# Performance work log

Measured on AMD Instinct MI355X. Metric: run time of the kernel, lower is better.

## Reference

```python
import jax, jax.numpy as jnp
import numpy as np

S, LC = 4096, 16
N_WORD, N_CHAR = 100000, 128
CHAR_DIM, CHAR_HIDDEN = 64, 128
N_DIM, N_HIDDEN, N_TAG = 256, 512, 64


def setup_inputs() -> dict:
    key = jax.random.key(0)
    ks = jax.random.split(key, 16)
    rn = lambda k, shape, s=0.1: (jax.random.normal(k, shape, jnp.float32) * s)
    inp = {
        'char_emb': rn(ks[0], (N_CHAR, CHAR_DIM), 1.0),
        'char_Wih': rn(ks[1], (4 * CHAR_HIDDEN, CHAR_DIM)),
        'char_Whh': rn(ks[2], (4 * CHAR_HIDDEN, CHAR_HIDDEN)),
        'char_bih': rn(ks[3], (4 * CHAR_HIDDEN,)),
        'char_bhh': rn(ks[4], (4 * CHAR_HIDDEN,)),
        'word_emb': rn(ks[5], (N_WORD, N_DIM), 1.0),
        'Wih': rn(ks[6], (4 * N_HIDDEN, N_DIM + CHAR_HIDDEN)),
        'Whh': rn(ks[7], (4 * N_HIDDEN, N_HIDDEN)),
        'bih': rn(ks[8], (4 * N_HIDDEN,)),
        'bhh': rn(ks[9], (4 * N_HIDDEN,)),
        'W1': rn(ks[10], (N_TAG, N_HIDDEN)),
        'b1': rn(ks[11], (N_TAG,)),
        'x': jax.random.randint(ks[12], (S,), 0, N_WORD),
        'chars': jax.random.randint(ks[13], (S, LC), 0, N_CHAR),
        'char_lens': jax.random.randint(ks[14], (S,), 1, LC + 1),
    }
    return inp


def _lstm(xs, mask, Wih, Whh, bih, bhh):
    # xs: [T, B, In], mask: [T, B] bool. PyTorch gate order: i, f, g, o.
    T, B, _ = xs.shape
    H = Whh.shape[1]
    def step(carry, inp):
        h, c = carry
        x_t, m_t = inp
        g = x_t @ Wih.T + bih + h @ Whh.T + bhh  # [B, 4H]
        i, f, gg, o = jnp.split(g, 4, axis=-1)
        c_new = jax.nn.sigmoid(f) * c + jax.nn.sigmoid(i) * jnp.tanh(gg)
        h_new = jax.nn.sigmoid(o) * jnp.tanh(c_new)
        m = m_t[:, None]
        h2 = jnp.where(m, h_new, h)
        c2 = jnp.where(m, c_new, c)
        return (h2, c2), h2
    init = (jnp.zeros((B, H), xs.dtype), jnp.zeros((B, H), xs.dtype))
    (h_fin, _), hs = jax.lax.scan(step, init, (xs, mask))
    return hs, h_fin


def reference(char_emb, char_Wih, char_Whh, char_bih, char_bhh,
              word_emb, Wih, Whh, bih, bhh, W1, b1,
              x, chars, char_lens):
    # --- char-level LSTM, all S words batched (replaces per-word Python loop) ---
    cx = char_emb[chars]                      # [S, LC, char_dim]
    cx = jnp.transpose(cx, (1, 0, 2))         # [LC, S, char_dim]
    cmask = jnp.arange(LC)[:, None] < char_lens[None, :]  # [LC, S]
    _, char_h = _lstm(cx, cmask, char_Wih, char_Whh, char_bih, char_bhh)  # [S, char_hidden]

    # --- word-level LSTM over the sentence (batch 1, as in original) ---
    wx = word_emb[x]                          # [S, n_dim]
    feat = jnp.concatenate([wx, char_h], axis=-1)[:, None, :]  # [S, 1, n_dim+char_hidden]
    wmask = jnp.ones((feat.shape[0], 1), bool)
    hs, _ = _lstm(feat, wmask, Wih, Whh, bih, bhh)  # [S, 1, n_hidden]
    hs = hs[:, 0, :]

    logits = hs @ W1.T + b1                   # [S, n_tag]
    return jax.nn.log_softmax(logits, axis=-1)
```

## Files before the change

### kernel.cpp

```cpp
#include <hip/hip_runtime.h>
#include <hip/hip_bf16.h>


#define OFF_FLAG  0
#define OFF_CEMB  16
#define OFF_CWIH  8208
#define OFF_CBIH  40976
#define OFF_CBHH  41488
#define OFF_CWHH  42000
#define OFF_BIH   107536
#define OFF_BHH   109584
#define OFF_W1T   111632
#define OFF_CGE   144400
#define OFF_CH    209936
#define OFF_XP2   734224
#define OFF_HH    4928528

#define SENT 0xFFFFFFFFu

__device__ __forceinline__ float sigf(float x) { return 1.0f / (1.0f + __expf(-x)); }
__device__ __forceinline__ float tanh_f(float x) { return 2.0f * sigf(2.0f * x) - 1.0f; }
__device__ __forceinline__ float b2f_lo(unsigned u) { return __uint_as_float(u << 16); }
__device__ __forceinline__ float b2f_hi(unsigned u) { return __uint_as_float(u & 0xFFFF0000u); }

__global__ void detect_kernel(const unsigned* __restrict__ w, int* __restrict__ flagp) {
    unsigned v = w[threadIdx.x];
    unsigned e = (v >> 7) & 0xFF;
    int inr = (e >= 100 && e <= 140) ? 1 : 0;
    unsigned long long m = __ballot(inr);
    if (threadIdx.x == 0) flagp[0] = (__popcll(m) >= 56) ? 1 : 0;
}

__global__ void convf_kernel(const void* __restrict__ s, float* __restrict__ d,
                             int n, const int* __restrict__ flagp) {
    int i = blockIdx.x * 256 + threadIdx.x;
    if (i >= n) return;
    d[i] = flagp[0] ? __bfloat162float(((const __hip_bfloat16*)s)[i])
                    : ((const float*)s)[i];
}

__global__ void w1t_kernel(const void* __restrict__ W1, float* __restrict__ W1T,
                           const int* __restrict__ flagp) {
    int i = blockIdx.x * 256 + threadIdx.x;
    int j = i & 63, k = i >> 6;
    W1T[i] = flagp[0] ? __bfloat162float(((const __hip_bfloat16*)W1)[j * 512 + k])
                      : ((const float*)W1)[j * 512 + k];
}

__global__ void __launch_bounds__(256) cge_kernel(
    const float* __restrict__ cemb, const float* __restrict__ cWih,
    const float* __restrict__ cbih, const float* __restrict__ cbhh,
    float* __restrict__ cge)
{
    __shared__ float xe[64];
    int c = blockIdx.x, tid = threadIdx.x;
    if (tid < 64) xe[tid] = cemb[c * 64 + tid];
    __syncthreads();
#pragma unroll
    for (int rep = 0; rep < 2; ++rep) {
        int j = rep * 256 + tid;
        float acc = cbih[j] + cbhh[j];
#pragma unroll 8
        for (int k = 0; k < 64; ++k)
            acc += xe[k] * cWih[j * 64 + k];
        cge[c * 512 + j] = acc;
    }
}

__global__ void __launch_bounds__(256) char_lstm_kernel(
    const float* __restrict__ cge, const float* __restrict__ Whh,
    const int* __restrict__ chars, const int* __restrict__ lens,
    float* __restrict__ char_h)
{
    __shared__ float hls[16][128];
    int tid = threadIdx.x;
    int wl = tid >> 4, sl = tid & 15;
    int w = blockIdx.x * 16 + wl;
    int len = lens[w];
    const int* cw = chars + w * 16;
    float c[8];
#pragma unroll
    for (int q = 0; q < 8; ++q) { c[q] = 0.0f; hls[wl][sl * 8 + q] = 0.0f; }

    for (int t = 0; t < 16; ++t) {
        __syncthreads();
        int ch = cw[t];
        const float* xg = cge + ch * 512;
        float acc[4][8];
#pragma unroll
        for (int g = 0; g < 4; ++g)
#pragma unroll
            for (int q = 0; q < 8; ++q)
                acc[g][q] = xg[g * 128 + sl * 8 + q];

        const float4* h4 = (const float4*)hls[wl];
#pragma unroll
        for (int g = 0; g < 4; ++g) {
            const float4* wbase = ((const float4*)Whh) + (g * 128 + sl * 8) * 32;
            for (int k4 = 0; k4 < 32; ++k4) {
                float4 hv = h4[k4];
#pragma unroll
                for (int q = 0; q < 8; ++q) {
                    float4 wv = wbase[q * 32 + k4];
                    acc[g][q] += wv.x * hv.x + wv.y * hv.y + wv.z * hv.z + wv.w * hv.w;
                }
            }
        }
        __syncthreads();
        if (t < len) {
#pragma unroll
            for (int q = 0; q < 8; ++q) {
                float iv = sigf(acc[0][q]);
                float fv = sigf(acc[1][q]);
                float gv = tanh_f(acc[2][q]);
                float ov = sigf(acc[3][q]);
                c[q] = fv * c[q] + iv * gv;
                hls[wl][sl * 8 + q] = ov * tanh_f(c[q]);
            }
        }
    }
    __syncthreads();
#pragma unroll
    for (int q = 0; q < 8; ++q)
        char_h[w * 128 + sl * 8 + q] = hls[wl][sl * 8 + q];
}

__global__ void __launch_bounds__(256) xp2_kernel(
    const void* __restrict__ wemb, const int* __restrict__ x,
    const float* __restrict__ char_h, const void* __restrict__ Wraw,
    const float* __restrict__ bih, const float* __restrict__ bhh,
    __hip_bfloat16* __restrict__ xp2, const int* __restrict__ flagp)
{
    __shared__ float feat[16][384];
    int flag = flagp[0];
    int tid = threadIdx.x, tl = tid >> 4, sl = tid & 15;
    int t = blockIdx.x * 16 + tl;
    int xw = x[t];
    for (int idx = sl; idx < 384; idx += 16) {
        float v;
        if (idx < 256)
            v = flag ? __bfloat162float(((const __hip_bfloat16*)wemb)[(size_t)xw * 256 + idx])
                     : ((const float*)wemb)[(size_t)xw * 256 + idx];
        else
            v = char_h[t * 128 + (idx - 256)];
        feat[tl][idx] = v;
    }
    __syncthreads();

    const float4* f4 = (const float4*)feat[tl];
    for (int rb = 0; rb < 4; ++rb) {
        int r0 = rb * 512 + sl * 32;
        for (int qc = 0; qc < 4; ++qc) {
            int rr = r0 + qc * 8;
            float acc[8];
#pragma unroll
            for (int q = 0; q < 8; ++q)
                acc[q] = bih[rr + q] + bhh[rr + q];
            if (!flag) {
                const float4* wb = ((const float4*)Wraw) + (size_t)rr * 96;
                for (int k4 = 0; k4 < 96; ++k4) {
                    float4 fv = f4[k4];
#pragma unroll
                    for (int q = 0; q < 8; ++q) {
                        float4 wv = wb[q * 96 + k4];
                        acc[q] += wv.x * fv.x + wv.y * fv.y + wv.z * fv.z + wv.w * fv.w;
                    }
                }
            } else {
                const uint2* wb = ((const uint2*)Wraw) + (size_t)rr * 96;
                for (int k4 = 0; k4 < 96; ++k4) {
                    float4 fv = f4[k4];
#pragma unroll
                    for (int q = 0; q < 8; ++q) {
                        uint2 wv = wb[q * 96 + k4];
                        acc[q] += b2f_lo(wv.x) * fv.x + b2f_hi(wv.x) * fv.y
                                + b2f_lo(wv.y) * fv.z + b2f_hi(wv.y) * fv.w;
                    }
                }
            }
#pragma unroll
            for (int q = 0; q < 8; ++q)
                xp2[(size_t)t * 2048 + rr + q] = __float2bfloat16(acc[q]);
        }
    }
}

__global__ void __launch_bounds__(1024, 4) word_lstm_kernel(
    const __hip_bfloat16* __restrict__ xp2, const void* __restrict__ Whh_raw,
    float* __restrict__ h_hist, const int* __restrict__ flagp)
{
    __shared__ float hpad[2][576];
    __shared__ float hout[16];
    __shared__ int step_flag;
    int flag = flagp[0];
    int wg = blockIdx.x;
    int tid = threadIdx.x;
    int wave = tid >> 6, lane = tid & 63;
    int g = lane >> 4, kk = lane & 15;
    int slot = wg * 16 + wave;
    int grow = g * 512 + slot;

    float4 wreg[8];
    if (!flag) {
        const float4* wr = (const float4*)((const float*)Whh_raw + (size_t)grow * 512 + kk * 32);
#pragma unroll
        for (int i = 0; i < 8; ++i) wreg[i] = wr[i];
    } else {
        const uint2* wr = (const uint2*)((const unsigned short*)Whh_raw + (size_t)grow * 512 + kk * 32);
#pragma unroll
        for (int i = 0; i < 8; ++i) {
            uint2 u = wr[i];
            wreg[i] = make_float4(b2f_lo(u.x), b2f_hi(u.x), b2f_lo(u.y), b2f_hi(u.y));
        }
    }

    for (int i = tid; i < 576; i += 1024) hpad[0][i] = 0.0f;
    if (tid == 0) step_flag = 0;
    __syncthreads();

    unsigned* hview = (unsigned*)h_hist;
    float c = 0.0f;

    for (int t = 0; t < 4096; ++t) {
        float xv = __bfloat162float(xp2[(size_t)t * 2048 + grow]);

        unsigned ls = 0;
        while (__hip_atomic_load(&step_flag, __ATOMIC_ACQUIRE,
                                 __HIP_MEMORY_SCOPE_WORKGROUP) < t) {
            if (++ls > (1u << 24)) break;
        }

        const float4* h4 = (const float4*)(&hpad[t & 1][kk * 36]);
        float acc = 0.0f;
#pragma unroll
        for (int i = 0; i < 8; ++i) {
            float4 hv = h4[i];
            acc += wreg[i].x * hv.x + wreg[i].y * hv.y +
                   wreg[i].z * hv.z + wreg[i].w * hv.w;
        }
        acc += __shfl_xor(acc, 1);
        acc += __shfl_xor(acc, 2);
        acc += __shfl_xor(acc, 4);
        acc += __shfl_xor(acc, 8);
        float gvt = acc + xv;

        float iv = __shfl(gvt, kk);
        float fv = __shfl(gvt, 16 + kk);
        float gg = __shfl(gvt, 32 + kk);
        float ov = __shfl(gvt, 48 + kk);
        c = sigf(fv) * c + sigf(iv) * tanh_f(gg);
        float h = sigf(ov) * tanh_f(c);

        if (lane == 0) hout[wave] = h;
        __syncthreads();

        if (wave == 0) {
            if (lane < 16)
                __hip_atomic_store(hview + (size_t)t * 512 + wg * 16 + lane,
                                   __float_as_uint(hout[lane]),
                                   __ATOMIC_RELAXED, __HIP_MEMORY_SCOPE_AGENT);

            if (t < 4095) {
                unsigned v[8];
                if ((lane >> 1) == wg) {
#pragma unroll
                    for (int i = 0; i < 8; ++i)
                        v[i] = __float_as_uint(hout[(lane & 1) * 8 + i]);
                } else {
                    const unsigned* src = hview + (size_t)t * 512 + lane * 8;
                    unsigned spins = 0;
                    bool bail = false;
                    for (;;) {
#pragma unroll
                        for (int i = 0; i < 8; ++i)
                            v[i] = __hip_atomic_load(src + i, __ATOMIC_RELAXED,
                                                     __HIP_MEMORY_SCOPE_AGENT);
                        int ok = 1;
#pragma unroll
                        for (int i = 0; i < 8; ++i) ok &= (v[i] != SENT);
                        if (ok) break;
                        if (++spins > (1u << 22)) { bail = true; break; }
                    }
                    if (bail) {
#pragma unroll
                        for (int i = 0; i < 8; ++i) v[i] = __float_as_uint(12345.0f);
                    }
                }
                float* dst = &hpad[(t + 1) & 1][(lane >> 2) * 36 + (lane & 3) * 8];
                ((float4*)dst)[0] = make_float4(__uint_as_float(v[0]), __uint_as_float(v[1]),
                                                __uint_as_float(v[2]), __uint_as_float(v[3]));
                ((float4*)dst)[1] = make_float4(__uint_as_float(v[4]), __uint_as_float(v[5]),
                                                __uint_as_float(v[6]), __uint_as_float(v[7]));
                __hip_atomic_store(&step_flag, t + 1, __ATOMIC_RELEASE,
                                   __HIP_MEMORY_SCOPE_WORKGROUP);
            }
        }
    }
}

__global__ void __launch_bounds__(64) out_kernel(
    const float* __restrict__ h_hist, const float* __restrict__ W1T,
    const void* __restrict__ b1raw, void* __restrict__ out,
    const int* __restrict__ flagp)
{
    __shared__ float hb[512];
    int flag = flagp[0];
    int t = blockIdx.x, j = threadIdx.x;
    const float4* src = (const float4*)(h_hist + (size_t)t * 512);
    ((float4*)hb)[j * 2] = src[j * 2];
    ((float4*)hb)[j * 2 + 1] = src[j * 2 + 1];
    __syncthreads();

    float acc = flag ? __bfloat162float(((const __hip_bfloat16*)b1raw)[j])
                     : ((const float*)b1raw)[j];
#pragma unroll 8
    for (int k = 0; k < 512; ++k)
        acc += hb[k] * W1T[k * 64 + j];

    float m = acc;
#pragma unroll
    for (int o = 32; o; o >>= 1) m = fmaxf(m, __shfl_xor(m, o));
    float e = __expf(acc - m);
    float s = e;
#pragma unroll
    for (int o = 32; o; o >>= 1) s += __shfl_xor(s, o);
    float r = acc - m - __logf(s);
    if (flag) ((__hip_bfloat16*)out)[t * 64 + j] = __float2bfloat16(r);
    else      ((float*)out)[t * 64 + j] = r;
}

extern "C" void kernel_launch(void* const* d_in, const int* in_sizes, int n_in,
                              void* d_out, int out_size, void* d_ws, size_t ws_size,
                              hipStream_t stream)
{
    (void)in_sizes; (void)n_in; (void)out_size; (void)ws_size;
    const void* char_emb = d_in[0];
    const void* char_Wih = d_in[1];
    const void* char_Whh = d_in[2];
    const void* char_bih = d_in[3];
    const void* char_bhh = d_in[4];
    const void* word_emb = d_in[5];
    const void* Wih      = d_in[6];
    const void* Whh      = d_in[7];
    const void* bih      = d_in[8];
    const void* bhh      = d_in[9];
    const void* W1       = d_in[10];
    const void* b1       = d_in[11];
    const int* x     = (const int*)d_in[12];
    const int* chars = (const int*)d_in[13];
    const int* lens  = (const int*)d_in[14];

    float* ws    = (float*)d_ws;
    int*   flagp = (int*)(ws + OFF_FLAG);
    float* cembf = ws + OFF_CEMB;
    float* cWihf = ws + OFF_CWIH;
    float* cbihf = ws + OFF_CBIH;
    float* cbhhf = ws + OFF_CBHH;
    float* cWhhf = ws + OFF_CWHH;
    float* bihf  = ws + OFF_BIH;
    float* bhhf  = ws + OFF_BHH;
    float* W1T   = ws + OFF_W1T;
    float* cge   = ws + OFF_CGE;
    float* charh = ws + OFF_CH;
    __hip_bfloat16* xp2 = (__hip_bfloat16*)(ws + OFF_XP2);
    float* hh    = ws + OFF_HH;

    hipMemsetAsync(hh, 0xFF, (size_t)4096 * 512 * 4, stream);

    detect_kernel<<<1, 64, 0, stream>>>((const unsigned*)char_emb, flagp);

    convf_kernel<<<(8192 + 255) / 256, 256, 0, stream>>>(char_emb, cembf, 8192, flagp);
    convf_kernel<<<(32768 + 255) / 256, 256, 0, stream>>>(char_Wih, cWihf, 32768, flagp);
    convf_kernel<<<2, 256, 0, stream>>>(char_bih, cbihf, 512, flagp);
    convf_kernel<<<2, 256, 0, stream>>>(char_bhh, cbhhf, 512, flagp);
    convf_kernel<<<(65536 + 255) / 256, 256, 0, stream>>>(char_Whh, cWhhf, 65536, flagp);
    convf_kernel<<<8, 256, 0, stream>>>(bih, bihf, 2048, flagp);
    convf_kernel<<<8, 256, 0, stream>>>(bhh, bhhf, 2048, flagp);
    w1t_kernel<<<128, 256, 0, stream>>>(W1, W1T, flagp);

    cge_kernel<<<128, 256, 0, stream>>>(cembf, cWihf, cbihf, cbhhf, cge);
    char_lstm_kernel<<<256, 256, 0, stream>>>(cge, cWhhf, chars, lens, charh);
    xp2_kernel<<<256, 256, 0, stream>>>(word_emb, x, charh, Wih, bihf, bhhf, xp2, flagp);
    word_lstm_kernel<<<32, 1024, 0, stream>>>(xp2, Whh, hh, flagp);
    out_kernel<<<4096, 64, 0, stream>>>(hh, W1T, b1, d_out, flagp);
}
```

Measured before the change: 13.50 ms.

## Co-locate word LSTM workgroups on one XCC and sync through shared L2

Launches 256 workgroups and keeps only the 16 that land on the same XCC as the first one (read via s_getreg), so the sequential word LSTM runs on 16 workgroups that share an L2. Each workgroup now handles 32 hidden units, two gate rows per thread. It probes whether workgroup-scope atomics are visible through the shared L2 and, if so, exchanges h with workgroup-scope stores and fetch_or reads, avoiding agent-scope coherence cost per step. Reductions use DPP row adds instead of shuffles, and the output projection is batched 16 timesteps per wave with bf16-packed W1 in LDS. The design depends on undocumented XCC placement and cache-coherence behaviour and can fall back or deadlock-bail, and packing W1 to bf16 loses precision.

```diff
diff --git a/kernel.cpp b/kernel.cpp
--- a/kernel.cpp
+++ b/kernel.cpp
@@ -2,26 +2,46 @@
 #include <hip/hip_bf16.h>
 
 
-#define OFF_FLAG  0
-#define OFF_CEMB  16
-#define OFF_CWIH  8208
-#define OFF_CBIH  40976
-#define OFF_CBHH  41488
-#define OFF_CWHH  42000
-#define OFF_BIH   107536
-#define OFF_BHH   109584
-#define OFF_W1T   111632
-#define OFF_CGE   144400
-#define OFF_CH    209936
-#define OFF_XP2   734224
-#define OFF_HH    4928528
+#define OFF_CTRLZ 0
+#define OFF_CTRLS 8
+#define OFF_FLAG  28
+#define OFF_CEMB  32
+#define OFF_CWIH  8224
+#define OFF_CBIH  40992
+#define OFF_CBHH  41504
+#define OFF_CWHH  42016
+#define OFF_BIH   107552
+#define OFF_BHH   109600
+#define OFF_W1T   111648
+#define OFF_CGE   144416
+#define OFF_CH    209952
+#define OFF_XP2   734240
+#define OFF_HH    4928544
 
 #define SENT 0xFFFFFFFFu
+#define XCC_GETREG_IMM 63508
 
 __device__ __forceinline__ float sigf(float x) { return 1.0f / (1.0f + __expf(-x)); }
 __device__ __forceinline__ float tanh_f(float x) { return 2.0f * sigf(2.0f * x) - 1.0f; }
 __device__ __forceinline__ float b2f_lo(unsigned u) { return __uint_as_float(u << 16); }
 __device__ __forceinline__ float b2f_hi(unsigned u) { return __uint_as_float(u & 0xFFFF0000u); }
+
+__device__ __forceinline__ unsigned l2_read(unsigned* p, unsigned oz) {
+    return __hip_atomic_fetch_or(p, oz, __ATOMIC_RELAXED, __HIP_MEMORY_SCOPE_WORKGROUP);
+}
+
+template <int CTRL>
+__device__ __forceinline__ float dpp_add(float x) {
+    int t = __builtin_amdgcn_update_dpp(0, __float_as_int(x), CTRL, 0xF, 0xF, true);
+    return x + __int_as_float(t);
+}
+__device__ __forceinline__ float row16_sum(float x) {
+    x = dpp_add<0x128>(x);
+    x = dpp_add<0x124>(x);
+    x = dpp_add<0x4E>(x);
+    x = dpp_add<0xB1>(x);
+    return x;
+}
 
 __global__ void detect_kernel(const unsigned* __restrict__ w, int* __restrict__ flagp) {
     unsigned v = w[threadIdx.x];
@@ -187,101 +207,176 @@
 
 __global__ void __launch_bounds__(1024, 4) word_lstm_kernel(
     const __hip_bfloat16* __restrict__ xp2, const void* __restrict__ Whh_raw,
-    float* __restrict__ h_hist, const int* __restrict__ flagp)
+    float* __restrict__ h_hist, const int* __restrict__ flagp,
+    int* __restrict__ cz, unsigned* __restrict__ cs)
 {
     __shared__ float hpad[2][576];
-    __shared__ float hout[16];
+    __shared__ float h_lds[32];
     __shared__ int step_flag;
+    __shared__ int dead_flag;
+    __shared__ int s_rank, s_mode;
+
+    int tid = threadIdx.x;
+    unsigned oz = (unsigned)cz[6];
+
+    if (tid == 0) {
+        int xcc = (int)(__builtin_amdgcn_s_getreg(XCC_GETREG_IMM) & 15u);
+        int e = __hip_atomic_fetch_add(&cz[0], 1, __ATOMIC_RELAXED, __HIP_MEMORY_SCOPE_AGENT);
+        if (e == 0)
+            __hip_atomic_store(&cs[0], (unsigned)xcc, __ATOMIC_RELEASE, __HIP_MEMORY_SCOPE_AGENT);
+        unsigned tgt; unsigned sp = 0;
+        do { tgt = __hip_atomic_load(&cs[0], __ATOMIC_ACQUIRE, __HIP_MEMORY_SCOPE_AGENT); }
+        while (tgt == SENT && ++sp < (1u << 20));
+        int rank = -1;
+        if (tgt != SENT && (unsigned)xcc == tgt) {
+            rank = __hip_atomic_fetch_add(&cz[1], 1, __ATOMIC_RELAXED, __HIP_MEMORY_SCOPE_AGENT);
+            if (rank >= 16) rank = -1;
+        }
+        s_rank = rank;
+        dead_flag = 0;
+    }
+    __syncthreads();
+    int rank = s_rank;
+    if (rank < 0) return;
+
+    if (tid == 0) {
+        __hip_atomic_store(&cs[1 + rank], 0xC0DE0000u + (unsigned)rank,
+                           __ATOMIC_RELAXED, __HIP_MEMORY_SCOPE_WORKGROUP);
+        int ok = 1;
+        for (int r = 0; r < 16 && ok; ++r) {
+            unsigned want = 0xC0DE0000u + (unsigned)r, v = 0; int sp2 = 0;
+            do { v = l2_read(&cs[1 + r], oz); } while (v != want && ++sp2 < 20000);
+            if (v != want) ok = 0;
+        }
+        if (!ok) __hip_atomic_fetch_or(&cz[3], 1, __ATOMIC_RELAXED, __HIP_MEMORY_SCOPE_AGENT);
+        __hip_atomic_fetch_add(&cz[2], 1, __ATOMIC_RELEASE, __HIP_MEMORY_SCOPE_AGENT);
+        unsigned sp3 = 0;
+        while (__hip_atomic_load(&cz[2], __ATOMIC_ACQUIRE, __HIP_MEMORY_SCOPE_AGENT) < 16
+               && ++sp3 < (1u << 20)) {}
+        s_mode = (__hip_atomic_load(&cz[3], __ATOMIC_RELAXED, __HIP_MEMORY_SCOPE_AGENT) == 0) ? 1 : 0;
+    }
+
     int flag = flagp[0];
-    int wg = blockIdx.x;
-    int tid = threadIdx.x;
     int wave = tid >> 6, lane = tid & 63;
-    int g = lane >> 4, kk = lane & 15;
-    int slot = wg * 16 + wave;
-    int grow = g * 512 + slot;
-
-    float4 wreg[8];
+    int slot_local = tid >> 5;
+    int p = tid & 31;
+    int gp = p >> 4, kk = p & 15;
+    int slot = rank * 32 + slot_local;
+    int r0 = (gp * 2) * 512 + slot;
+    int r1 = (gp * 2 + 1) * 512 + slot;
+
+    float4 w0[8], w1[8];
     if (!flag) {
-        const float4* wr = (const float4*)((const float*)Whh_raw + (size_t)grow * 512 + kk * 32);
-#pragma unroll
-        for (int i = 0; i < 8; ++i) wreg[i] = wr[i];
+        const float4* a = (const float4*)((const float*)Whh_raw + (size_t)r0 * 512 + kk * 32);
+        const float4* b = (const float4*)((const float*)Whh_raw + (size_t)r1 * 512 + kk * 32);
+#pragma unroll
+        for (int i = 0; i < 8; ++i) { w0[i] = a[i]; w1[i] = b[i]; }
     } else {
-        const uint2* wr = (const uint2*)((const unsigned short*)Whh_raw + (size_t)grow * 512 + kk * 32);
+        const uint2* a = (const uint2*)((const unsigned short*)Whh_raw + (size_t)r0 * 512 + kk * 32);
+        const uint2* b = (const uint2*)((const unsigned short*)Whh_raw + (size_t)r1 * 512 + kk * 32);
 #pragma unroll
         for (int i = 0; i < 8; ++i) {
-            uint2 u = wr[i];
-            wreg[i] = make_float4(b2f_lo(u.x), b2f_hi(u.x), b2f_lo(u.y), b2f_hi(u.y));
+            uint2 ua = a[i], ub = b[i];
+            w0[i] = make_float4(b2f_lo(ua.x), b2f_hi(ua.x), b2f_lo(ua.y), b2f_hi(ua.y));
+            w1[i] = make_float4(b2f_lo(ub.x), b2f_hi(ub.x), b2f_lo(ub.y), b2f_hi(ub.y));
         }
     }
 
     for (int i = tid; i < 576; i += 1024) hpad[0][i] = 0.0f;
     if (tid == 0) step_flag = 0;
     __syncthreads();
+    int l2mode = s_mode;
 
     unsigned* hview = (unsigned*)h_hist;
     float c = 0.0f;
 
     for (int t = 0; t < 4096; ++t) {
-        float xv = __bfloat162float(xp2[(size_t)t * 2048 + grow]);
-
-        unsigned ls = 0;
-        while (__hip_atomic_load(&step_flag, __ATOMIC_ACQUIRE,
-                                 __HIP_MEMORY_SCOPE_WORKGROUP) < t) {
-            if (++ls > (1u << 24)) break;
+        float xv0 = __bfloat162float(xp2[(size_t)t * 2048 + r0]);
+        float xv1 = __bfloat162float(xp2[(size_t)t * 2048 + r1]);
+
+        if (__hip_atomic_load(&dead_flag, __ATOMIC_RELAXED, __HIP_MEMORY_SCOPE_WORKGROUP) == 0) {
+            unsigned ls = 0;
+            while (__hip_atomic_load(&step_flag, __ATOMIC_ACQUIRE,
+                                     __HIP_MEMORY_SCOPE_WORKGROUP) < t) {
+                if (++ls > (1u << 22)) {
+                    __hip_atomic_store(&dead_flag, 1, __ATOMIC_RELAXED, __HIP_MEMORY_SCOPE_WORKGROUP);
+                    break;
+                }
+            }
         }
 
         const float4* h4 = (const float4*)(&hpad[t & 1][kk * 36]);
-        float acc = 0.0f;
+        float a0 = 0.0f, a1 = 0.0f;
 #pragma unroll
         for (int i = 0; i < 8; ++i) {
             float4 hv = h4[i];
-            acc += wreg[i].x * hv.x + wreg[i].y * hv.y +
-                   wreg[i].z * hv.z + wreg[i].w * hv.w;
-        }
-        acc += __shfl_xor(acc, 1);
-        acc += __shfl_xor(acc, 2);
-        acc += __shfl_xor(acc, 4);
-        acc += __shfl_xor(acc, 8);
-        float gvt = acc + xv;
-
-        float iv = __shfl(gvt, kk);
-        float fv = __shfl(gvt, 16 + kk);
-        float gg = __shfl(gvt, 32 + kk);
-        float ov = __shfl(gvt, 48 + kk);
+            a0 += w0[i].x * hv.x + w0[i].y * hv.y + w0[i].z * hv.z + w0[i].w * hv.w;
+            a1 += w1[i].x * hv.x + w1[i].y * hv.y + w1[i].z * hv.z + w1[i].w * hv.w;
+        }
+        a0 = row16_sum(a0) + xv0;
+        a1 = row16_sum(a1) + xv1;
+        float o0 = __shfl_xor(a0, 16);
+        float o1 = __shfl_xor(a1, 16);
+        float iv = gp ? o0 : a0;
+        float fv = gp ? o1 : a1;
+        float gg = gp ? a0 : o0;
+        float ov = gp ? a1 : o1;
         c = sigf(fv) * c + sigf(iv) * tanh_f(gg);
         float h = sigf(ov) * tanh_f(c);
 
-        if (lane == 0) hout[wave] = h;
+        if (p == 0) h_lds[slot_local] = h;
         __syncthreads();
 
         if (wave == 0) {
-            if (lane < 16)
-                __hip_atomic_store(hview + (size_t)t * 512 + wg * 16 + lane,
-                                   __float_as_uint(hout[lane]),
-                                   __ATOMIC_RELAXED, __HIP_MEMORY_SCOPE_AGENT);
-
+            if (lane < 32) {
+                unsigned hv = __float_as_uint(h_lds[lane]);
+                unsigned* dstp = hview + (size_t)t * 512 + rank * 32 + lane;
+                if (l2mode)
+                    __hip_atomic_store(dstp, hv, __ATOMIC_RELAXED, __HIP_MEMORY_SCOPE_WORKGROUP);
+                else
+                    __hip_atomic_store(dstp, hv, __ATOMIC_RELAXED, __HIP_MEMORY_SCOPE_AGENT);
+            }
             if (t < 4095) {
                 unsigned v[8];
-                if ((lane >> 1) == wg) {
+                if ((lane >> 2) == rank) {
 #pragma unroll
                     for (int i = 0; i < 8; ++i)
-                        v[i] = __float_as_uint(hout[(lane & 1) * 8 + i]);
+                        v[i] = __float_as_uint(h_lds[(lane & 3) * 8 + i]);
                 } else {
-                    const unsigned* src = hview + (size_t)t * 512 + lane * 8;
-                    unsigned spins = 0;
-                    bool bail = false;
-                    for (;;) {
-#pragma unroll
-                        for (int i = 0; i < 8; ++i)
-                            v[i] = __hip_atomic_load(src + i, __ATOMIC_RELAXED,
-                                                     __HIP_MEMORY_SCOPE_AGENT);
-                        int ok = 1;
-#pragma unroll
-                        for (int i = 0; i < 8; ++i) ok &= (v[i] != SENT);
-                        if (ok) break;
-                        if (++spins > (1u << 22)) { bail = true; break; }
+                    int deadv = __hip_atomic_load(&dead_flag, __ATOMIC_RELAXED,
+                                                  __HIP_MEMORY_SCOPE_WORKGROUP);
+                    bool bail = (deadv != 0);
+                    if (!bail) {
+                        unsigned* src = hview + (size_t)t * 512 + lane * 8;
+                        unsigned spins = 0;
+                        if (l2mode) {
+                            for (;;) {
+#pragma unroll
+                                for (int i = 0; i < 8; ++i)
+                                    v[i] = l2_read(src + i, oz);
+                                int ok = 1;
+#pragma unroll
+                                for (int i = 0; i < 8; ++i) ok &= (v[i] != SENT);
+                                if (ok) break;
+                                if (++spins > (1u << 16)) { bail = true; break; }
+                            }
+                        } else {
+                            for (;;) {
+#pragma unroll
+                                for (int i = 0; i < 8; ++i)
+                                    v[i] = __hip_atomic_load(src + i, __ATOMIC_RELAXED,
+                                                             __HIP_MEMORY_SCOPE_AGENT);
+                                int ok = 1;
+#pragma unroll
+                                for (int i = 0; i < 8; ++i) ok &= (v[i] != SENT);
+                                if (ok) break;
+                                if (++spins > (1u << 16)) { bail = true; break; }
+                            }
+                        }
                     }
                     if (bail) {
+                        __hip_atomic_store(&dead_flag, 1, __ATOMIC_RELAXED,
+                                           __HIP_MEMORY_SCOPE_WORKGROUP);
 #pragma unroll
                         for (int i = 0; i < 8; ++i) v[i] = __float_as_uint(12345.0f);
                     }
@@ -298,35 +393,63 @@
     }
 }
 
-__global__ void __launch_bounds__(64) out_kernel(
+__global__ void __launch_bounds__(256) out_kernel(
     const float* __restrict__ h_hist, const float* __restrict__ W1T,
     const void* __restrict__ b1raw, void* __restrict__ out,
     const int* __restrict__ flagp)
 {
-    __shared__ float hb[512];
-    int flag = flagp[0];
-    int t = blockIdx.x, j = threadIdx.x;
-    const float4* src = (const float4*)(h_hist + (size_t)t * 512);
-    ((float4*)hb)[j * 2] = src[j * 2];
-    ((float4*)hb)[j * 2 + 1] = src[j * 2 + 1];
-    __syncthreads();
-
-    float acc = flag ? __bfloat162float(((const __hip_bfloat16*)b1raw)[j])
+    __shared__ unsigned wlds[128 * 64];
+    __shared__ float hb[4][256];
+    int flagv = flagp[0];
+    int tid = threadIdx.x, wv = tid >> 6, j = tid & 63;
+    int t0 = blockIdx.x * 64 + wv * 16;
+
+    float bj = flagv ? __bfloat162float(((const __hip_bfloat16*)b1raw)[j])
                      : ((const float*)b1raw)[j];
-#pragma unroll 8
-    for (int k = 0; k < 512; ++k)
-        acc += hb[k] * W1T[k * 64 + j];
-
-    float m = acc;
-#pragma unroll
-    for (int o = 32; o; o >>= 1) m = fmaxf(m, __shfl_xor(m, o));
-    float e = __expf(acc - m);
-    float s = e;
-#pragma unroll
-    for (int o = 32; o; o >>= 1) s += __shfl_xor(s, o);
-    float r = acc - m - __logf(s);
-    if (flag) ((__hip_bfloat16*)out)[t * 64 + j] = __float2bfloat16(r);
-    else      ((float*)out)[t * 64 + j] = r;
+    float acc[16];
+#pragma unroll
+    for (int i = 0; i < 16; ++i) acc[i] = bj;
+
+    for (int pass = 0; pass < 2; ++pass) {
+        __syncthreads();
+        for (int i = tid; i < 128 * 64; i += 256) {
+            int q = i >> 6, j2 = i & 63;
+            int k = pass * 256 + q * 2;
+            unsigned lo = (__float_as_uint(W1T[k * 64 + j2]) + 0x8000u) >> 16;
+            unsigned hi = (__float_as_uint(W1T[(k + 1) * 64 + j2]) + 0x8000u) & 0xFFFF0000u;
+            wlds[i] = hi | lo;
+        }
+        __syncthreads();
+        for (int ti = 0; ti < 16; ++ti) {
+            int t = t0 + ti;
+            const float4* hsrc = (const float4*)(h_hist + (size_t)t * 512 + pass * 256);
+            ((float4*)hb[wv])[j] = hsrc[j];
+            __syncthreads();
+            float a = acc[ti];
+            const float2* hb2 = (const float2*)hb[wv];
+#pragma unroll 16
+            for (int q = 0; q < 128; ++q) {
+                float2 hv = hb2[q];
+                unsigned wp = wlds[q * 64 + j];
+                a += b2f_lo(wp) * hv.x + b2f_hi(wp) * hv.y;
+            }
+            acc[ti] = a;
+            __syncthreads();
+        }
+    }
+
+#pragma unroll
+    for (int ti = 0; ti < 16; ++ti) {
+        int t = t0 + ti;
+        float a = acc[ti];
+        float m = a;
+        for (int o = 32; o; o >>= 1) m = fmaxf(m, __shfl_xor(m, o));
+        float e = __expf(a - m), s = e;
+        for (int o = 32; o; o >>= 1) s += __shfl_xor(s, o);
+        float r = a - m - __logf(s);
+        if (flagv) ((__hip_bfloat16*)out)[t * 64 + j] = __float2bfloat16(r);
+        else       ((float*)out)[t * 64 + j] = r;
+    }
 }
 
 extern "C" void kernel_launch(void* const* d_in, const int* in_sizes, int n_in,
@@ -351,6 +474,8 @@
     const int* lens  = (const int*)d_in[14];
 
     float* ws    = (float*)d_ws;
+    int*      cz = (int*)(ws + OFF_CTRLZ);
+    unsigned* cs = (unsigned*)(ws + OFF_CTRLS);
     int*   flagp = (int*)(ws + OFF_FLAG);
     float* cembf = ws + OFF_CEMB;
     float* cWihf = ws + OFF_CWIH;
@@ -365,6 +490,8 @@
     __hip_bfloat16* xp2 = (__hip_bfloat16*)(ws + OFF_XP2);
     float* hh    = ws + OFF_HH;
 
+    hipMemsetAsync(cz, 0, 8 * 4, stream);
+    hipMemsetAsync(cs, 0xFF, 20 * 4, stream);
     hipMemsetAsync(hh, 0xFF, (size_t)4096 * 512 * 4, stream);
 
     detect_kernel<<<1, 64, 0, stream>>>((const unsigned*)char_emb, flagp);
@@ -381,6 +508,6 @@
     cge_kernel<<<128, 256, 0, stream>>>(cembf, cWihf, cbihf, cbhhf, cge);
     char_lstm_kernel<<<256, 256, 0, stream>>>(cge, cWhhf, chars, lens, charh);
     xp2_kernel<<<256, 256, 0, stream>>>(word_emb, x, charh, Wih, bihf, bhhf, xp2, flagp);
-    word_lstm_kernel<<<32, 1024, 0, stream>>>(xp2, Whh, hh, flagp);
-    out_kernel<<<4096, 64, 0, stream>>>(hh, W1T, b1, d_out, flagp);
-}
+    word_lstm_kernel<<<256, 1024, 0, stream>>>(xp2, Whh, hh, flagp, cz, cs);
+    out_kernel<<<64, 256, 0, stream>>>(hh, W1T, b1, d_out, flagp);
+}
```

After: 28.23 ms. +109.1%, slower.
